# Kernel optimization log

Hardware: AMD Instinct MI355X
Metric: run time of the kernel (lower is better)

The kernel has to match this reference:

```python
import jax, jax.numpy as jnp
import numpy as np

N, C_IN, H, W = 48, 64, 128, 128


def _conv3x3(x, w, b):
    # NCHW conv, kernel 3, stride 1, pad 1 (SAME)
    y = jax.lax.conv_general_dilated(
        x, w, window_strides=(1, 1), padding=((1, 1), (1, 1)),
        dimension_numbers=("NCHW", "OIHW", "NCHW"))
    return y + b[None, :, None, None]


def setup_inputs() -> dict:
    key = jax.random.key(0)
    ks = jax.random.split(key, 4)
    s1 = 1.0 / np.sqrt(C_IN * 9)
    s2 = 1.0 / np.sqrt(128 * 9)
    s3 = 1.0 / np.sqrt(32 * 9)
    return {
        "x": jax.random.normal(ks[0], (N, C_IN, H, W), dtype=jnp.float32),
        "to_process": jnp.arange(N, dtype=jnp.int64) if jax.config.jax_enable_x64 else jnp.arange(N, dtype=jnp.int32),
        "batch_size": 8,
        "W1": jax.random.normal(ks[1], (128, C_IN, 3, 3), dtype=jnp.float32) * s1,
        "b1": jnp.zeros((128,), dtype=jnp.float32),
        "W2": jax.random.normal(ks[2], (32, 128, 3, 3), dtype=jnp.float32) * s2,
        "b2": jnp.zeros((32,), dtype=jnp.float32),
        "W3": jax.random.normal(ks[3], (1, 32, 3, 3), dtype=jnp.float32) * s3,
        "b3": jnp.zeros((1,), dtype=jnp.float32),
    }


def reference(x, to_process, batch_size, W1, b1, W2, b2, W3, b3):
    # x holds only the active sites listed in to_process; all ops are per-site.
    x = jax.nn.relu(_conv3x3(x, W1, b1))          # [N,128,H,W]
    x = jax.nn.relu(_conv3x3(x, W2, b2))          # [N,32,H,W]
    n, c, h, w = x.shape
    # SparseBilinearUpsample(2): half-pixel-center bilinear x2 (align_corners=False)
    x = jax.image.resize(x, (n, c, 2 * h, 2 * w), method="bilinear")
    x = _conv3x3(x, W3, b3)                        # [N,1,2H,2W]
    return x
```

## Files before the change

### kernel.cpp

```cpp
#include <hip/hip_runtime.h>


typedef _Float16 half_t;
typedef _Float16 half2_t __attribute__((ext_vector_type(2)));
typedef _Float16 half4_t __attribute__((ext_vector_type(4)));
typedef _Float16 half8   __attribute__((ext_vector_type(8)));
typedef float    floatx4  __attribute__((ext_vector_type(4)));
typedef float    floatx16 __attribute__((ext_vector_type(16)));

__global__ __launch_bounds__(256) void repack_w(
    const float* __restrict__ W1, const float* __restrict__ W2,
    const float* __restrict__ W3, half_t* __restrict__ wh1,
    half_t* __restrict__ wh2, half_t* __restrict__ wh3)
{
    int idx = blockIdx.x * 256 + threadIdx.x;
    if (idx < 73728) {
        int ci = idx & 63, co = (idx >> 6) & 127, tap = idx >> 13;
        wh1[idx] = (half_t)W1[(co * 64 + ci) * 9 + tap];
    } else if (idx < 110592) {
        int j = idx - 73728;
        int ci = j & 127, co = (j >> 7) & 31, tap = j >> 12;
        wh2[j] = (half_t)W2[(co * 128 + ci) * 9 + tap];
    } else if (idx < 110880) {
        int j = idx - 110592;
        int ci = j & 31, tap = j >> 5;
        wh3[j] = (half_t)W3[ci * 9 + tap];
    }
}

__global__ __launch_bounds__(256) void repack_x(
    const float* __restrict__ x, half_t* __restrict__ xh)
{
    const int tid = threadIdx.x;
    const int px = tid & 127, rr = tid >> 7;
    const int y = blockIdx.x * 2 + rr;
    const int n = blockIdx.y;
    const float* xn = x + (size_t)n * 64 * 16384 + (size_t)y * 128 + px;
    half2_t hb[32];
#pragma unroll
    for (int c2 = 0; c2 < 32; ++c2) {
        float f0 = xn[(size_t)(2 * c2) * 16384];
        float f1 = xn[(size_t)(2 * c2 + 1) * 16384];
        half2_t h; h.x = (half_t)f0; h.y = (half_t)f1;
        hb[c2] = h;
    }
    half_t* op = xh + (((size_t)n * 128 + y) * 128 + px) * 64;
#pragma unroll
    for (int k = 0; k < 8; ++k)
        *(half8*)(op + k * 8) = *(half8*)(&hb[k * 4]);
}

__global__ __launch_bounds__(256, 2) void conv1_mfma(
    const half_t* __restrict__ xh,
    const half_t* __restrict__ wh,
    const float*  __restrict__ bias,
    half_t* __restrict__ y1h)
{
    __shared__ half_t lx[10 * 34 * 72];
    const int tid  = threadIdx.x;
    const int lane = tid & 63;
    const int wave = tid >> 6;
    const int l31 = lane & 31, lq = lane >> 5;
    const int wco = wave >> 1, wpx = wave & 1;
    const int x0 = blockIdx.x * 32, y0 = blockIdx.y * 8;
    const int n = blockIdx.z;
    const half_t* xn = xh + (size_t)n * (128 * 128 * 64);

    half8 st[11];
#pragma unroll
    for (int k = 0; k < 11; ++k) {
        int idx = tid + k * 256;
        half8 v = {};
        if (idx < 10 * 34 * 8) {
            int ch = idx & 7;
            int p  = idx >> 3;
            int col = p % 34, row = p / 34;
            int gx = x0 - 1 + col, gy = y0 - 1 + row;
            if ((unsigned)gx < 128u && (unsigned)gy < 128u)
                v = *(const half8*)(xn + ((size_t)gy * 128 + gx) * 64 + ch * 8);
        }
        st[k] = v;
    }
#pragma unroll
    for (int k = 0; k < 11; ++k) {
        int idx = tid + k * 256;
        if (idx < 10 * 34 * 8) {
            int ch = idx & 7;
            int p  = idx >> 3;
            int col = p % 34, row = p / 34;
            *(half8*)(&lx[(row * 34 + col) * 72 + ch * 8]) = st[k];
        }
    }
    __syncthreads();

    floatx16 acc[2][4] = {};

#pragma unroll
    for (int tap = 0; tap < 9; ++tap) {
        const int dy = tap / 3, dx = tap % 3;
        const half_t* wt = wh + tap * (128 * 64) + (wco * 64 + l31) * 64 + lq * 8;
        const half_t* bp = &lx[((wpx * 4 + dy) * 34 + l31 + dx) * 72 + lq * 8];
#pragma unroll
        for (int kc = 0; kc < 4; ++kc) {
            half8 a0 = *(const half8*)(wt + kc * 16);
            half8 a1 = *(const half8*)(wt + 32 * 64 + kc * 16);
            half8 b[4];
#pragma unroll
            for (int nf = 0; nf < 4; ++nf)
                b[nf] = *(const half8*)(bp + nf * (34 * 72) + kc * 16);
#pragma unroll
            for (int nf = 0; nf < 4; ++nf) {
                acc[0][nf] = __builtin_amdgcn_mfma_f32_32x32x16_f16(a0, b[nf], acc[0][nf], 0, 0, 0);
                acc[1][nf] = __builtin_amdgcn_mfma_f32_32x32x16_f16(a1, b[nf], acc[1][nf], 0, 0, 0);
            }
        }
    }

#pragma unroll
    for (int mf = 0; mf < 2; ++mf) {
        int co0 = wco * 64 + mf * 32 + lq * 4;
        int q = wco * 2 + mf;
#pragma unroll
        for (int nf = 0; nf < 4; ++nf) {
            floatx16 A = acc[mf][nf];
            int oy = y0 + wpx * 4 + nf, ox = x0 + l31;
            half_t* op = y1h + ((((size_t)n * 4 + q) * 16384) + oy * 128 + ox) * 32 + lq * 4;
#pragma unroll
            for (int g = 0; g < 4; ++g) {
                floatx4 bv = *(const floatx4*)(bias + co0 + 8 * g);
                half4_t o;
                o.x = (half_t)fmaxf(A[4 * g + 0] + bv.x, 0.f);
                o.y = (half_t)fmaxf(A[4 * g + 1] + bv.y, 0.f);
                o.z = (half_t)fmaxf(A[4 * g + 2] + bv.z, 0.f);
                o.w = (half_t)fmaxf(A[4 * g + 3] + bv.w, 0.f);
                *(half4_t*)(op + 8 * g) = o;
            }
        }
    }
}

__global__ __launch_bounds__(256, 3) void conv2_mfma(
    const half_t* __restrict__ y1h,
    const half_t* __restrict__ wh,
    const float*  __restrict__ bias,
    half_t* __restrict__ y2h)
{
    __shared__ half_t lx[4][19][34][8];
    const int tid  = threadIdx.x;
    const int lane = tid & 63;
    const int w    = tid >> 6;
    const int l15 = lane & 15, quad = lane >> 4;
    const int x0 = blockIdx.x * 32, y0 = blockIdx.y * 16;
    const int n = blockIdx.z;

    floatx4 acc[2][8] = {};

    for (int h = 0; h < 4; ++h) {
        const half_t* yn = y1h + ((size_t)n * 4 + h) * (16384 * 32);
        half8 st[10];
#pragma unroll
        for (int k = 0; k < 10; ++k) {
            int idx = tid + k * 256;
            half8 v = {};
            if (idx < 18 * 34 * 4) {
                int ch = idx & 3;
                int p  = idx >> 2;
                int col = p % 34, row = p / 34;
                int gx = x0 - 1 + col, gy = y0 - 1 + row;
                if ((unsigned)gx < 128u && (unsigned)gy < 128u)
                    v = *(const half8*)(yn + ((size_t)gy * 128 + gx) * 32 + ch * 8);
            }
            st[k] = v;
        }
#pragma unroll
        for (int k = 0; k < 10; ++k) {
            int idx = tid + k * 256;
            if (idx < 18 * 34 * 4) {
                int ch = idx & 3;
                int p  = idx >> 2;
                int col = p % 34, row = p / 34;
                *(half8*)(&lx[ch][row][col][0]) = st[k];
            }
        }
        __syncthreads();
#pragma unroll
        for (int tap = 0; tap < 9; ++tap) {
            const int dy = tap / 3, dx = tap % 3;
            const half_t* wt = wh + tap * (32 * 128) + l15 * 128 + h * 32 + quad * 8;
            half8 a0 = *(const half8*)(wt);
            half8 a1 = *(const half8*)(wt + 16 * 128);
#pragma unroll
            for (int nf = 0; nf < 8; ++nf) {
                int rr = w * 4 + (nf >> 1) + dy;
                int cc = (nf & 1) * 16 + l15 + dx;
                half8 b = *(const half8*)(&lx[quad][rr][cc][0]);
                acc[0][nf] = __builtin_amdgcn_mfma_f32_16x16x32_f16(a0, b, acc[0][nf], 0, 0, 0);
                acc[1][nf] = __builtin_amdgcn_mfma_f32_16x16x32_f16(a1, b, acc[1][nf], 0, 0, 0);
            }
        }
        __syncthreads();
    }

#pragma unroll
    for (int mf = 0; mf < 2; ++mf) {
        int co0 = mf * 16 + quad * 4;
        floatx4 bv = *(const floatx4*)(bias + co0);
#pragma unroll
        for (int nf = 0; nf < 8; ++nf) {
            int oy = y0 + w * 4 + (nf >> 1), ox = x0 + (nf & 1) * 16 + l15;
            floatx4 A = acc[mf][nf];
            half4_t o;
            o.x = (half_t)fmaxf(A.x + bv.x, 0.f);
            o.y = (half_t)fmaxf(A.y + bv.y, 0.f);
            o.z = (half_t)fmaxf(A.z + bv.z, 0.f);
            o.w = (half_t)fmaxf(A.w + bv.w, 0.f);
            *(half4_t*)(y2h + (((size_t)n * 128 + oy) * 128 + ox) * 32 + co0) = o;
        }
    }
}

__global__ __launch_bounds__(256) void conv3_fused(
    const half_t* __restrict__ y2h,
    const half_t* __restrict__ wh3,
    const float*  __restrict__ bias,
    float* __restrict__ out)
{
    __shared__ half_t lu[18 * 34 * 40];
    const int tid = threadIdx.x;
    const int c = tid & 31, r = tid >> 5;
    const int x0 = blockIdx.x * 32, y0 = blockIdx.y * 16;
    const int n = blockIdx.z;
    const half_t* base = y2h + (size_t)n * (128 * 128 * 32);

    half8 st[10];
#pragma unroll
    for (int k = 0; k < 10; ++k) {
        int idx = tid + k * 256;
        half8 o = {};
        if (idx < 18 * 34 * 4) {
            int cc = idx & 3;
            int p  = idx >> 2;
            int col = p % 34, row = p / 34;
            int X = x0 - 1 + col, Y = y0 - 1 + row;
            if ((unsigned)X < 256u && (unsigned)Y < 256u) {
                int jx = X >> 1, jy = Y >> 1;
                int jxo = (X & 1) ? (jx < 127 ? jx + 1 : 127) : (jx > 0 ? jx - 1 : 0);
                int jyo = (Y & 1) ? (jy < 127 ? jy + 1 : 127) : (jy > 0 ? jy - 1 : 0);
                const half_t* p00 = base + ((size_t)jy  * 128 + jx ) * 32 + cc * 8;
                const half_t* p01 = base + ((size_t)jy  * 128 + jxo) * 32 + cc * 8;
                const half_t* p10 = base + ((size_t)jyo * 128 + jx ) * 32 + cc * 8;
                const half_t* p11 = base + ((size_t)jyo * 128 + jxo) * 32 + cc * 8;
                half8 v00 = *(const half8*)p00;
                half8 v01 = *(const half8*)p01;
                half8 v10 = *(const half8*)p10;
                half8 v11 = *(const half8*)p11;
                o = v00 * (half_t)0.5625f + (v01 + v10) * (half_t)0.1875f
                  + v11 * (half_t)0.0625f;
            }
        }
        st[k] = o;
    }
#pragma unroll
    for (int k = 0; k < 10; ++k) {
        int idx = tid + k * 256;
        if (idx < 18 * 34 * 4) {
            int cc = idx & 3;
            int p  = idx >> 2;
            int col = p % 34, row = p / 34;
            *(half8*)(&lu[(row * 34 + col) * 40 + cc * 8]) = st[k];
        }
    }
    __syncthreads();

#pragma unroll
    for (int s = 0; s < 2; ++s) {
        float acc = 0.f;
#pragma unroll
        for (int tap = 0; tap < 9; ++tap) {
            const int dy = tap / 3, dx = tap % 3;
            const half_t* lp = &lu[((s * 8 + r + dy) * 34 + c + dx) * 40];
            const half_t* wp = wh3 + tap * 32;
#pragma unroll
            for (int cc = 0; cc < 4; ++cc) {
                half8 v = *(const half8*)(lp + cc * 8);
                half8 w = *(const half8*)(wp + cc * 8);
                acc = __builtin_amdgcn_fdot2(__builtin_shufflevector(v, v, 0, 1),
                                             __builtin_shufflevector(w, w, 0, 1), acc, false);
                acc = __builtin_amdgcn_fdot2(__builtin_shufflevector(v, v, 2, 3),
                                             __builtin_shufflevector(w, w, 2, 3), acc, false);
                acc = __builtin_amdgcn_fdot2(__builtin_shufflevector(v, v, 4, 5),
                                             __builtin_shufflevector(w, w, 4, 5), acc, false);
                acc = __builtin_amdgcn_fdot2(__builtin_shufflevector(v, v, 6, 7),
                                             __builtin_shufflevector(w, w, 6, 7), acc, false);
            }
        }
        out[((size_t)n * 256 + (y0 + s * 8 + r)) * 256 + x0 + c] = acc + bias[0];
    }
}

extern "C" void kernel_launch(void* const* d_in, const int* in_sizes, int n_in,
                              void* d_out, int out_size, void* d_ws, size_t ws_size,
                              hipStream_t stream) {
    const float* x  = (const float*)d_in[0];
    const float* W1 = (const float*)d_in[3];
    const float* b1 = (const float*)d_in[4];
    const float* W2 = (const float*)d_in[5];
    const float* b2 = (const float*)d_in[6];
    const float* W3 = (const float*)d_in[7];
    const float* b3 = (const float*)d_in[8];
    float* out = (float*)d_out;

    char* ws = (char*)d_ws;
    half_t* xh  = (half_t*)ws;
    half_t* y1h = (half_t*)(ws + 201326592ull);
    half_t* y2h = (half_t*)(ws + 402653184ull);
    half_t* wh1 = (half_t*)(ws + 452984832ull);
    half_t* wh2 = wh1 + 73728;
    half_t* wh3 = wh2 + 36864;

    repack_w<<<434, 256, 0, stream>>>(W1, W2, W3, wh1, wh2, wh3);
    repack_x<<<dim3(64, 48), 256, 0, stream>>>(x, xh);
    conv1_mfma<<<dim3(4, 16, 48), 256, 0, stream>>>(xh, wh1, b1, y1h);
    conv2_mfma<<<dim3(4, 8, 48), 256, 0, stream>>>(y1h, wh2, b2, y2h);
    conv3_fused<<<dim3(8, 16, 48), 256, 0, stream>>>(y2h, wh3, b3, out);
}
```

Baseline: 721.1 us.

## Pad conv1 input in global memory and stage tiles via direct global-to-LDS loads

The NHWC fp16 input buffer is now stored with a zeroed one-pixel border, written by a new kernel, so conv1 no longer needs bounds checks when loading its halo tile. The tile is copied straight into LDS with global_load_lds instead of going through registers, using an XOR swizzle on the 16-byte chunks in place of the padded row stride. The MFMA B-operand reads apply the matching swizzle. This is meant to cut register pressure and load instruction overhead in conv1, at the cost of an extra small kernel launch and a larger workspace footprint. It also relies on the padded buffer fitting before the y1h offset.

```diff
diff --git a/kernel.cpp b/kernel.cpp
--- a/kernel.cpp
+++ b/kernel.cpp
@@ -7,6 +7,9 @@
 typedef _Float16 half8   __attribute__((ext_vector_type(8)));
 typedef float    floatx4  __attribute__((ext_vector_type(4)));
 typedef float    floatx16 __attribute__((ext_vector_type(16)));
+
+typedef const __attribute__((address_space(1))) char* gptr_t;
+typedef __attribute__((address_space(3))) char* lptr_t;
 
 __global__ __launch_bounds__(256) void repack_w(
     const float* __restrict__ W1, const float* __restrict__ W2,
@@ -28,6 +31,24 @@
     }
 }
 
+__global__ __launch_bounds__(256) void zero_border(half_t* __restrict__ xh)
+{
+    const int n = blockIdx.x;
+    half_t* base = xh + (size_t)n * (132 * 130 * 64);
+    for (int i = threadIdx.x; i < 516; i += 256) {
+        int gy, gx;
+        if (i < 130)      { gy = 0;   gx = i; }
+        else if (i < 260) { gy = 129; gx = i - 130; }
+        else if (i < 388) { gy = i - 260 + 1; gx = 0; }
+        else              { gy = i - 388 + 1; gx = 129; }
+        half8 z = {};
+        half_t* p = base + ((size_t)gy * 130 + gx) * 64;
+#pragma unroll
+        for (int k = 0; k < 8; ++k)
+            *(half8*)(p + k * 8) = z;
+    }
+}
+
 __global__ __launch_bounds__(256) void repack_x(
     const float* __restrict__ x, half_t* __restrict__ xh)
 {
@@ -44,7 +65,7 @@
         half2_t h; h.x = (half_t)f0; h.y = (half_t)f1;
         hb[c2] = h;
     }
-    half_t* op = xh + (((size_t)n * 128 + y) * 128 + px) * 64;
+    half_t* op = xh + (((size_t)n * 132 + (y + 1)) * 130 + (px + 1)) * 64;
 #pragma unroll
     for (int k = 0; k < 8; ++k)
         *(half8*)(op + k * 8) = *(half8*)(&hb[k * 4]);
@@ -56,7 +77,7 @@
     const float*  __restrict__ bias,
     half_t* __restrict__ y1h)
 {
-    __shared__ half_t lx[10 * 34 * 72];
+    __shared__ half_t lx[352 * 64];
     const int tid  = threadIdx.x;
     const int lane = tid & 63;
     const int wave = tid >> 6;
@@ -64,32 +85,17 @@
     const int wco = wave >> 1, wpx = wave & 1;
     const int x0 = blockIdx.x * 32, y0 = blockIdx.y * 8;
     const int n = blockIdx.z;
-    const half_t* xn = xh + (size_t)n * (128 * 128 * 64);
-
-    half8 st[11];
+    const half_t* xn = xh + (size_t)n * (132 * 130 * 64);
+
 #pragma unroll
     for (int k = 0; k < 11; ++k) {
         int idx = tid + k * 256;
-        half8 v = {};
-        if (idx < 10 * 34 * 8) {
-            int ch = idx & 7;
-            int p  = idx >> 3;
-            int col = p % 34, row = p / 34;
-            int gx = x0 - 1 + col, gy = y0 - 1 + row;
-            if ((unsigned)gx < 128u && (unsigned)gy < 128u)
-                v = *(const half8*)(xn + ((size_t)gy * 128 + gx) * 64 + ch * 8);
-        }
-        st[k] = v;
-    }
-#pragma unroll
-    for (int k = 0; k < 11; ++k) {
-        int idx = tid + k * 256;
-        if (idx < 10 * 34 * 8) {
-            int ch = idx & 7;
-            int p  = idx >> 3;
-            int col = p % 34, row = p / 34;
-            *(half8*)(&lx[(row * 34 + col) * 72 + ch * 8]) = st[k];
-        }
+        int m = idx & 7, p = idx >> 3;
+        int row = p / 34, col = p - row * 34;
+        int sw = m ^ (p & 7);
+        const half_t* src = xn + ((size_t)(y0 + row) * 130 + (x0 + col)) * 64 + sw * 8;
+        half_t* dst = &lx[(size_t)(k * 256 + wave * 64) * 8];
+        __builtin_amdgcn_global_load_lds((gptr_t)src, (lptr_t)dst, 16, 0, 0);
     }
     __syncthreads();
 
@@ -99,15 +105,18 @@
     for (int tap = 0; tap < 9; ++tap) {
         const int dy = tap / 3, dx = tap % 3;
         const half_t* wt = wh + tap * (128 * 64) + (wco * 64 + l31) * 64 + lq * 8;
-        const half_t* bp = &lx[((wpx * 4 + dy) * 34 + l31 + dx) * 72 + lq * 8];
+        const int pr0 = (wpx * 4 + dy) * 34 + l31 + dx;
 #pragma unroll
         for (int kc = 0; kc < 4; ++kc) {
             half8 a0 = *(const half8*)(wt + kc * 16);
             half8 a1 = *(const half8*)(wt + 32 * 64 + kc * 16);
             half8 b[4];
 #pragma unroll
-            for (int nf = 0; nf < 4; ++nf)
-                b[nf] = *(const half8*)(bp + nf * (34 * 72) + kc * 16);
+            for (int nf = 0; nf < 4; ++nf) {
+                int p = pr0 + nf * 34;
+                int m = (kc * 2 + lq) ^ (p & 7);
+                b[nf] = *(const half8*)(&lx[p * 64 + m * 8]);
+            }
 #pragma unroll
             for (int nf = 0; nf < 4; ++nf) {
                 acc[0][nf] = __builtin_amdgcn_mfma_f32_32x32x16_f16(a0, b[nf], acc[0][nf], 0, 0, 0);
@@ -319,6 +328,7 @@
     half_t* wh3 = wh2 + 36864;
 
     repack_w<<<434, 256, 0, stream>>>(W1, W2, W3, wh1, wh2, wh3);
+    zero_border<<<48, 256, 0, stream>>>(xh);
     repack_x<<<dim3(64, 48), 256, 0, stream>>>(x, xh);
     conv1_mfma<<<dim3(4, 16, 48), 256, 0, stream>>>(xh, wh1, b1, y1h);
     conv2_mfma<<<dim3(4, 8, 48), 256, 0, stream>>>(y1h, wh2, b2, y2h);
```

Result: slower. 861.5 us (+19.5%).
